# Optimization experiments

Measured on AMD Instinct MI355X. Metric: run time of the kernel, lower is better.

## Reference

```python
import jax, jax.numpy as jnp
import numpy as np

EPS = 1e-6

def _rmsnorm(x, w):
    rms = jax.lax.rsqrt(jnp.mean(x * x, axis=-1, keepdims=True) + EPS)
    return x * rms * w

def setup_inputs() -> dict:
    key = jax.random.key(0)
    ks = jax.random.split(key, 4)
    BS, N, D, DI = 4, 8192, 1024, 2048
    x = jax.random.normal(ks[0], (BS, N, D), dtype=jnp.float32)
    h_prev = jax.random.normal(ks[1], (BS, DI), dtype=jnp.float32)
    norm_w = jnp.ones((D,), dtype=jnp.float32)
    W_in = jax.random.normal(ks[2], (2 * DI, D), dtype=jnp.float32) * (1.0 / np.sqrt(D))
    b_in = jnp.zeros((2 * DI,), dtype=jnp.float32)
    W_out = jax.random.normal(ks[3], (D, DI), dtype=jnp.float32) * (1.0 / np.sqrt(DI))
    b_out = jnp.zeros((D,), dtype=jnp.float32)
    return {"x": x, "h_prev": h_prev, "norm_w": norm_w, "W_in": W_in,
            "b_in": b_in, "W_out": W_out, "b_out": b_out}

def _scan(a, b, h0):
    # h_t = a_t * h_{t-1} + b_t ; fold h0 into first step
    b = b.at[:, 0].set(a[:, 0] * h0 + b[:, 0])
    def combine(c1, c2):
        a1, b1 = c1
        a2, b2 = c2
        return (a2 * a1, a2 * b1 + b2)
    _, h = jax.lax.associative_scan(combine, (a, b), axis=1)
    return h  # [BS, N, E]

def reference(x, h_prev, norm_w, W_in, b_in, W_out, b_out):
    DI = W_out.shape[1]
    xn = _rmsnorm(x, norm_w)
    ab = jnp.einsum('bnd,ed->bne', xn, W_in) + b_in  # [BS, N, 2*DI]
    a_raw, b_raw = ab[..., :DI], ab[..., DI:]
    a = jax.nn.sigmoid(a_raw)
    b = jax.nn.silu(b_raw)
    h = _scan(a, b, h_prev)  # [BS, N, DI]
    out = jnp.einsum('bne,de->bnd', h, W_out) + b_out + x
    return out, h[:, -1]
```

## Files before the change

### kernel.cpp

```cpp
#include <hip/hip_runtime.h>
#include <stdint.h>
#include <stddef.h>

typedef __bf16 bf16;
typedef __attribute__((ext_vector_type(8))) __bf16 bf16x8;
typedef __attribute__((ext_vector_type(4))) __bf16 bf16x4;
typedef __attribute__((ext_vector_type(4))) float floatx4;

#define DEV static __device__ __forceinline__

DEV void async_load16(const void* g, void* l) {
  __builtin_amdgcn_global_load_lds(
      (__attribute__((address_space(1))) void*)(g),
      (__attribute__((address_space(3))) void*)(l),
      16, 0, 0);
}

DEV float bf16lo_to_f(uint32_t pv) {
  uint32_t b = pv << 16; float f; __builtin_memcpy(&f, &b, 4); return f;
}
DEV float bf16hi_to_f(uint32_t pv) {
  uint32_t b = pv & 0xffff0000u; float f; __builtin_memcpy(&f, &b, 4); return f;
}

DEV int win_orig_row(int c) {
  int jt16 = c >> 4;
  int is_b = jt16 & 1;
  int p    = (jt16 >> 1) * 16 + (c & 15);
  return p + is_b * 2048;
}

__global__ __launch_bounds__(256)
void f2bf_kernel(const float* __restrict__ in, bf16* __restrict__ out, int n4)
{
  int i = blockIdx.x * 256 + threadIdx.x;
  if (i < n4) {
    float4 v = ((const float4*)in)[i];
    bf16x4 o = { (bf16)v.x, (bf16)v.y, (bf16)v.z, (bf16)v.w };
    ((bf16x4*)out)[i] = o;
  }
}

__global__ __launch_bounds__(256)
void f2bf_win_perm(const float* __restrict__ in, bf16* __restrict__ out)
{
  int c = blockIdx.x;
  int orig = win_orig_row(c);
  float4 v = ((const float4*)(in + (size_t)orig * 1024))[threadIdx.x];
  bf16x4 o = { (bf16)v.x, (bf16)v.y, (bf16)v.z, (bf16)v.w };
  ((bf16x4*)(out + (size_t)c * 1024))[threadIdx.x] = o;
}

__global__ __launch_bounds__(256)
void bias_perm_kernel(const float* __restrict__ b_in, float* __restrict__ biasP)
{
  int c = blockIdx.x * 256 + threadIdx.x;
  biasP[c] = b_in[win_orig_row(c)];
}

__global__ __launch_bounds__(256)
void rmsnorm_kernel(const float* __restrict__ x, const float* __restrict__ w,
                    bf16* __restrict__ xn)
{
  const int row = blockIdx.x;
  const int tid = threadIdx.x;
  float4 v = ((const float4*)(x + (size_t)row * 1024))[tid];
  float ss = v.x * v.x + v.y * v.y + v.z * v.z + v.w * v.w;
  #pragma unroll
  for (int off = 1; off < 64; off <<= 1)
    ss += __shfl_xor(ss, off, 64);
  __shared__ float red[4];
  if ((tid & 63) == 0) red[tid >> 6] = ss;
  __syncthreads();
  float tot = red[0] + red[1] + red[2] + red[3];
  float rms = rsqrtf(tot * (1.0f / 1024.0f) + 1e-6f);
  float4 wv = ((const float4*)w)[tid];
  bf16x4 o;
  o[0] = (bf16)(v.x * rms * wv.x);
  o[1] = (bf16)(v.y * rms * wv.y);
  o[2] = (bf16)(v.z * rms * wv.z);
  o[3] = (bf16)(v.w * rms * wv.w);
  ((bf16x4*)(xn + (size_t)row * 1024))[tid] = o;
}

template <int MODE>
__global__ __launch_bounds__(256)
void gemm_bt_kernel(const bf16* __restrict__ A, const bf16* __restrict__ B,
                    int N, int K, int numNt,
                    uint32_t* __restrict__ sbw, float* __restrict__ out,
                    const float* __restrict__ bias,
                    const float* __restrict__ resid)
{
  __shared__ bf16 ldsA[128 * 64];
  __shared__ bf16 ldsB[128 * 64];

  const int GROUP_M = 16;
  int bid = blockIdx.x;
  int per_group = GROUP_M * numNt;
  int group = bid / per_group;
  int rem = bid - group * per_group;
  int mt = group * GROUP_M + (rem % GROUP_M);
  int nt = rem / GROUP_M;
  const int m0 = mt * 128, n0 = nt * 128;

  const int tid  = threadIdx.x;
  const int lane = tid & 63;
  const int wave = tid >> 6;
  const int wm   = (wave & 1) * 64;
  const int wn   = (wave >> 1) * 64;
  const int l15  = lane & 15;
  const int quad = lane >> 4;

  floatx4 acc[4][4];
  #pragma unroll
  for (int i = 0; i < 4; ++i)
    #pragma unroll
    for (int j = 0; j < 4; ++j)
      acc[i][j] = (floatx4){0.f, 0.f, 0.f, 0.f};

  for (int kt = 0; kt < K; kt += 64) {
    #pragma unroll
    for (int i = 0; i < 4; ++i) {
      int c   = tid + i * 256;
      int row = c >> 3;
      int kgg = (c & 7) ^ (row & 7);
      async_load16(A + (size_t)(m0 + row) * K + kt + kgg * 8, &ldsA[c * 8]);
      async_load16(B + (size_t)(n0 + row) * K + kt + kgg * 8, &ldsB[c * 8]);
    }
    __syncthreads();
    #pragma unroll
    for (int ks = 0; ks < 2; ++ks) {
      bf16x8 af[4], bfr[4];
      #pragma unroll
      for (int i = 0; i < 4; ++i) {
        int row = wm + i * 16 + l15;
        int kg  = ks * 4 + quad;
        af[i]  = *(const bf16x8*)&ldsA[(row * 8 + (kg ^ (row & 7))) * 8];
        int col = wn + i * 16 + l15;
        bfr[i] = *(const bf16x8*)&ldsB[(col * 8 + (kg ^ (col & 7))) * 8];
      }
      #pragma unroll
      for (int i = 0; i < 4; ++i)
        #pragma unroll
        for (int j = 0; j < 4; ++j)
          acc[i][j] = __builtin_amdgcn_mfma_f32_16x16x32_bf16(af[i], bfr[j], acc[i][j], 0, 0, 0);
    }
    __syncthreads();
  }

  if (MODE == 1) {
    #pragma unroll
    for (int i = 0; i < 4; ++i) {
      #pragma unroll
      for (int pair = 0; pair < 2; ++pair) {
        int j0 = pair * 2;
        float bs = bias[n0 + wn + j0 * 16 + l15];
        float bb = bias[n0 + wn + j0 * 16 + 16 + l15];
        int ch = (n0 >> 1) + (wn >> 1) + pair * 16 + l15;
        #pragma unroll
        for (int r = 0; r < 4; ++r) {
          int row = m0 + wm + i * 16 + quad * 4 + r;
          float vs = acc[i][j0][r] + bs;
          float vb = acc[i][j0 + 1][r] + bb;
          float s  = 1.0f / (1.0f + __expf(vs));
          float sv = 1.0f / (1.0f + __expf(vb));
          float bv = vb - vb * sv;
          union { bf16 h[2]; uint32_t u; } pk;
          pk.h[0] = (bf16)s;
          pk.h[1] = (bf16)bv;
          sbw[(size_t)row * 2048 + ch] = pk.u;
        }
      }
    }
  } else {
    #pragma unroll
    for (int i = 0; i < 4; ++i) {
      #pragma unroll
      for (int j = 0; j < 4; ++j) {
        #pragma unroll
        for (int r = 0; r < 4; ++r) {
          int row = m0 + wm + i * 16 + quad * 4 + r;
          int col = n0 + wn + j * 16 + l15;
          float v = acc[i][j][r] + bias[col] + resid[(size_t)row * N + col];
          out[(size_t)row * N + col] = v;
        }
      }
    }
  }
}

__global__ __launch_bounds__(256)
void scan_phase1(const uint32_t* __restrict__ sb,
                 float* __restrict__ Ac, float* __restrict__ Bc)
{
  int g = blockIdx.x * 256 + threadIdx.x;
  int e     = g & 2047;
  int chunk = (g >> 11) & 31;
  int seq   = g >> 16;
  size_t base = ((size_t)(seq * 8192 + chunk * 256)) * 2048 + e;
  float A = 1.0f, Bv = 0.0f;
  #pragma unroll 8
  for (int n = 0; n < 256; ++n) {
    uint32_t pv = sb[base + (size_t)n * 2048];
    float a = 1.0f - bf16lo_to_f(pv);
    float b = bf16hi_to_f(pv);
    A *= a;
    Bv = a * Bv + b;
  }
  Ac[g] = A;
  Bc[g] = Bv;
}

__global__ __launch_bounds__(256)
void scan_phase2(const float* __restrict__ Ac, const float* __restrict__ Bc,
                 const float* __restrict__ h_prev,
                 float* __restrict__ carry, float* __restrict__ h_last)
{
  int g = blockIdx.x * 256 + threadIdx.x;
  int e = g & 2047;
  int seq = g >> 11;
  float h = h_prev[g];
  #pragma unroll
  for (int c = 0; c < 32; ++c) {
    size_t idx = ((size_t)(seq * 32 + c)) * 2048 + e;
    carry[idx] = h;
    h = Ac[idx] * h + Bc[idx];
  }
  h_last[g] = h;
}

__global__ __launch_bounds__(256)
void scan_phase3(const uint32_t* __restrict__ sb,
                 const float* __restrict__ carry, bf16* __restrict__ h_out)
{
  int g = blockIdx.x * 256 + threadIdx.x;
  int e     = g & 2047;
  int chunk = (g >> 11) & 31;
  int seq   = g >> 16;
  float h = carry[((size_t)(seq * 32 + chunk)) * 2048 + e];
  size_t base = ((size_t)(seq * 8192 + chunk * 256)) * 2048 + e;
  #pragma unroll 8
  for (int n = 0; n < 256; ++n) {
    uint32_t pv = sb[base + (size_t)n * 2048];
    float a = 1.0f - bf16lo_to_f(pv);
    float b = bf16hi_to_f(pv);
    h = a * h + b;
    h_out[base + (size_t)n * 2048] = (bf16)h;
  }
}

extern "C" void kernel_launch(void* const* d_in, const int* in_sizes, int n_in,
                              void* d_out, int out_size, void* d_ws, size_t ws_size,
                              hipStream_t stream)
{
  const float* x      = (const float*)d_in[0];
  const float* h_prev = (const float*)d_in[1];
  const float* norm_w = (const float*)d_in[2];
  const float* W_in   = (const float*)d_in[3];
  const float* b_in   = (const float*)d_in[4];
  const float* W_out  = (const float*)d_in[5];
  const float* b_out  = (const float*)d_in[6];

  float* out    = (float*)d_out;
  float* h_last = out + (size_t)33554432;

  int BSl = 4, passes = 1;
  {
    size_t need4 = 8388608 + 4194304 + 16384
                 + 3 * ((size_t)4 * 32 * 2048 * 4)
                 + (size_t)4 * 8192 * 2048 * 4
                 + (size_t)4 * 8192 * 1024 * 2
                 + (size_t)4 * 8192 * 2048 * 2;
    if (ws_size < need4) { BSl = 1; passes = 4; }
  }
  const size_t Mrows = (size_t)BSl * 8192;
  char* ws = (char*)d_ws;
  bf16*  Win_b  = (bf16*)(ws);
  bf16*  Wout_b = (bf16*)(ws + 8388608);
  float* biasP  = (float*)(ws + 12582912);
  size_t acN    = (size_t)BSl * 32 * 2048;
  char*  pa     = ws + 12599296;
  float* Ac     = (float*)(pa);
  float* Bc     = (float*)(pa + acN * 4);
  float* carry  = (float*)(pa + acN * 8);
  char*  p0     = pa + acN * 12;
  uint32_t* sbw = (uint32_t*)(p0);
  bf16*  xn     = (bf16*)(p0 + Mrows * 2048 * 4);
  bf16*  h_arr  = (bf16*)(p0 + Mrows * 2048 * 4 + Mrows * 1024 * 2);

  f2bf_win_perm<<<4096, 256, 0, stream>>>(W_in, Win_b);
  f2bf_kernel<<<2048, 256, 0, stream>>>(W_out, Wout_b, 2097152 / 4);
  bias_perm_kernel<<<16, 256, 0, stream>>>(b_in, biasP);

  for (int p = 0; p < passes; ++p) {
    const float* xp = x + (size_t)p * Mrows * 1024;

    rmsnorm_kernel<<<(int)Mrows, 256, 0, stream>>>(xp, norm_w, xn);

    int numMt = (int)(Mrows / 128);
    gemm_bt_kernel<1><<<numMt * 32, 256, 0, stream>>>(
        xn, Win_b, 4096, 1024, 32, sbw, nullptr, biasP, nullptr);

    scan_phase1<<<BSl * 256, 256, 0, stream>>>(sbw, Ac, Bc);
    scan_phase2<<<BSl * 8, 256, 0, stream>>>(Ac, Bc, h_prev + (size_t)p * BSl * 2048,
                                             carry, h_last + (size_t)p * BSl * 2048);
    scan_phase3<<<BSl * 256, 256, 0, stream>>>(sbw, carry, h_arr);

    gemm_bt_kernel<2><<<numMt * 8, 256, 0, stream>>>(
        h_arr, Wout_b, 1024, 2048, 8, nullptr, out + (size_t)p * Mrows * 1024,
        b_out, xp);
  }
}
```

Before: 968.2 us.

## Replace 128x128 GEMM with 256x256 eight-wave pipelined double-buffered kernel

Both GEMMs move from a 128x128 tile with 4 waves and a single LDS buffer to a 256x256 tile with 8 waves. The new kernel double-buffers A and B in 128 KB of LDS and interleaves async global-to-LDS loads with MFMA quadrants under explicit waitcnt and barrier control plus s_setprio. Block IDs are also remapped across XCDs with a smaller M group. The aim is to hide load latency behind compute and raise arithmetic intensity per tile. In exchange it uses more registers and LDS, relies on fragile hand-written vmcnt accounting, and launches fewer blocks.

```diff
diff --git a/kernel.cpp b/kernel.cpp
--- a/kernel.cpp
+++ b/kernel.cpp
@@ -83,85 +83,175 @@
   ((bf16x4*)(xn + (size_t)row * 1024))[tid] = o;
 }
 
+DEV void stage_half(const bf16* __restrict__ P, int ldk, int grow0, int kt,
+                    bf16* ldst, int tid)
+{
+  #pragma unroll
+  for (int s = 0; s < 2; ++s) {
+    int cc  = (s << 9) + tid;
+    int row = cc >> 3;
+    int kgg = (cc & 7) ^ (row & 7);
+    async_load16(P + (size_t)(grow0 + row) * ldk + kt + kgg * 8, ldst + cc * 8);
+  }
+}
+
+DEV bf16x8 ld_frag(const bf16* base, int r, int kg) {
+  return *(const bf16x8*)(base + (((r << 3) + (kg ^ (r & 7))) << 3));
+}
+
+#define FENCE asm volatile("" ::: "memory")
+#define BAR() do { FENCE; __builtin_amdgcn_s_barrier(); FENCE; } while (0)
+#define LGKM0 asm volatile("s_waitcnt lgkmcnt(0)" ::: "memory")
+#define VMC4  asm volatile("s_waitcnt vmcnt(4)" ::: "memory")
+#define VMC0  asm volatile("s_waitcnt vmcnt(0)" ::: "memory")
+
+#define LOADA(LAP, IH) \
+  _Pragma("unroll") \
+  for (int ii = 0; ii < 4; ++ii) { \
+    _Pragma("unroll") \
+    for (int ks = 0; ks < 2; ++ks) \
+      af[ii][ks] = ld_frag(LAP, ((IH)*4 + ii)*16 + l15, ks*4 + quad); \
+  }
+
+#define LOADB(LBP, JH) \
+  _Pragma("unroll") \
+  for (int jj = 0; jj < 2; ++jj) { \
+    _Pragma("unroll") \
+    for (int ks = 0; ks < 2; ++ks) \
+      bfr[(JH)*2 + jj][ks] = ld_frag(LBP, rBb + ((JH)*2 + jj)*16 + l15, ks*4 + quad); \
+  }
+
+#define MFMAQ(IH, JH) \
+  _Pragma("unroll") \
+  for (int ii = 0; ii < 4; ++ii) { \
+    _Pragma("unroll") \
+    for (int jj = 0; jj < 2; ++jj) { \
+      _Pragma("unroll") \
+      for (int ks = 0; ks < 2; ++ks) \
+        acc[(IH)*4+ii][(JH)*2+jj] = __builtin_amdgcn_mfma_f32_16x16x32_bf16( \
+            af[ii][ks], bfr[(JH)*2+jj][ks], acc[(IH)*4+ii][(JH)*2+jj], 0, 0, 0); \
+    } \
+  }
+
 template <int MODE>
-__global__ __launch_bounds__(256)
-void gemm_bt_kernel(const bf16* __restrict__ A, const bf16* __restrict__ B,
+__global__ __launch_bounds__(512, 2)
+void gemm256_kernel(const bf16* __restrict__ A, const bf16* __restrict__ B,
                     int N, int K, int numNt,
                     uint32_t* __restrict__ sbw, float* __restrict__ out,
                     const float* __restrict__ bias,
                     const float* __restrict__ resid)
 {
-  __shared__ bf16 ldsA[128 * 64];
-  __shared__ bf16 ldsB[128 * 64];
-
-  const int GROUP_M = 16;
+  __shared__ __align__(16) bf16 lds[65536];
+
+  int nwg = gridDim.x;
   int bid = blockIdx.x;
+  int cpx = nwg >> 3;
+  int wg  = (bid & 7) * cpx + (bid >> 3);
+  const int GROUP_M = 8;
   int per_group = GROUP_M * numNt;
-  int group = bid / per_group;
-  int rem = bid - group * per_group;
+  int group = wg / per_group;
+  int rem   = wg - group * per_group;
   int mt = group * GROUP_M + (rem % GROUP_M);
   int nt = rem / GROUP_M;
-  const int m0 = mt * 128, n0 = nt * 128;
+  const int m0 = mt * 256, n0 = nt * 256;
 
   const int tid  = threadIdx.x;
   const int lane = tid & 63;
   const int wave = tid >> 6;
-  const int wm   = (wave & 1) * 64;
-  const int wn   = (wave >> 1) * 64;
+  const int wm   = wave >> 2;
+  const int wn   = wave & 3;
+  const int wh   = wn >> 1;
+  const int rBb  = (wn & 1) * 64;
   const int l15  = lane & 15;
   const int quad = lane >> 4;
 
-  floatx4 acc[4][4];
+  const bf16* lA0 = lds +         wm * 8192;
+  const bf16* lA1 = lds + 16384 + wm * 8192;
+  const bf16* lB0 = lds + 32768 + wh * 8192;
+  const bf16* lB1 = lds + 49152 + wh * 8192;
+
+  floatx4 acc[8][4];
   #pragma unroll
-  for (int i = 0; i < 4; ++i)
+  for (int i = 0; i < 8; ++i)
     #pragma unroll
     for (int j = 0; j < 4; ++j)
       acc[i][j] = (floatx4){0.f, 0.f, 0.f, 0.f};
 
-  for (int kt = 0; kt < K; kt += 64) {
-    #pragma unroll
-    for (int i = 0; i < 4; ++i) {
-      int c   = tid + i * 256;
-      int row = c >> 3;
-      int kgg = (c & 7) ^ (row & 7);
-      async_load16(A + (size_t)(m0 + row) * K + kt + kgg * 8, &ldsA[c * 8]);
-      async_load16(B + (size_t)(n0 + row) * K + kt + kgg * 8, &ldsB[c * 8]);
-    }
-    __syncthreads();
-    #pragma unroll
-    for (int ks = 0; ks < 2; ++ks) {
-      bf16x8 af[4], bfr[4];
-      #pragma unroll
-      for (int i = 0; i < 4; ++i) {
-        int row = wm + i * 16 + l15;
-        int kg  = ks * 4 + quad;
-        af[i]  = *(const bf16x8*)&ldsA[(row * 8 + (kg ^ (row & 7))) * 8];
-        int col = wn + i * 16 + l15;
-        bfr[i] = *(const bf16x8*)&ldsB[(col * 8 + (kg ^ (col & 7))) * 8];
-      }
-      #pragma unroll
-      for (int i = 0; i < 4; ++i)
-        #pragma unroll
-        for (int j = 0; j < 4; ++j)
-          acc[i][j] = __builtin_amdgcn_mfma_f32_16x16x32_bf16(af[i], bfr[j], acc[i][j], 0, 0, 0);
-    }
-    __syncthreads();
+  bf16x8 af[4][2];
+  bf16x8 bfr[4][2];
+
+  stage_half(A, K, m0,       0, lds +     0, tid);
+  stage_half(A, K, m0 + 128, 0, lds +  8192, tid);
+  stage_half(B, K, n0,       0, lds + 32768, tid);
+  stage_half(B, K, n0 + 128, 0, lds + 40960, tid);
+  stage_half(B, K, n0,      64, lds + 49152, tid);
+  stage_half(B, K, n0 + 128,64, lds + 57344, tid);
+  VMC4;
+  BAR();
+
+  const int U = K >> 7;
+  for (int u = 0; u < U; ++u) {
+    const int k1 = (u << 7) + 64;
+    const int k2 = (u << 7) + 128;
+    const int k3 = (u << 7) + 192;
+    const bool more = (u + 1 < U);
+
+    LOADA(lA0, 0); LOADB(lB0, 0);
+    stage_half(A, K, m0, k1, lds + 16384, tid);
+    BAR(); LGKM0;
+    __builtin_amdgcn_s_setprio(1); MFMAQ(0, 0); __builtin_amdgcn_s_setprio(0);
+    BAR();
+    LOADB(lB0, 1);
+    stage_half(A, K, m0 + 128, k1, lds + 24576, tid);
+    BAR(); LGKM0;
+    __builtin_amdgcn_s_setprio(1); MFMAQ(0, 1); __builtin_amdgcn_s_setprio(0);
+    BAR();
+    LOADA(lA0, 1);
+    if (more) stage_half(B, K, n0, k2, lds + 32768, tid);
+    BAR(); LGKM0;
+    __builtin_amdgcn_s_setprio(1); MFMAQ(1, 0); __builtin_amdgcn_s_setprio(0);
+    BAR();
+    if (more) stage_half(B, K, n0 + 128, k2, lds + 40960, tid);
+    BAR(); LGKM0;
+    __builtin_amdgcn_s_setprio(1); MFMAQ(1, 1); __builtin_amdgcn_s_setprio(0);
+    if (more) { VMC4; } else { VMC0; }
+    BAR();
+    LOADA(lA1, 0); LOADB(lB1, 0);
+    if (more) stage_half(A, K, m0, k2, lds + 0, tid);
+    BAR(); LGKM0;
+    __builtin_amdgcn_s_setprio(1); MFMAQ(0, 0); __builtin_amdgcn_s_setprio(0);
+    BAR();
+    LOADB(lB1, 1);
+    if (more) stage_half(A, K, m0 + 128, k2, lds + 8192, tid);
+    BAR(); LGKM0;
+    __builtin_amdgcn_s_setprio(1); MFMAQ(0, 1); __builtin_amdgcn_s_setprio(0);
+    BAR();
+    LOADA(lA1, 1);
+    if (more) stage_half(B, K, n0, k3, lds + 49152, tid);
+    BAR(); LGKM0;
+    __builtin_amdgcn_s_setprio(1); MFMAQ(1, 0); __builtin_amdgcn_s_setprio(0);
+    BAR();
+    if (more) stage_half(B, K, n0 + 128, k3, lds + 57344, tid);
+    BAR(); LGKM0;
+    __builtin_amdgcn_s_setprio(1); MFMAQ(1, 1); __builtin_amdgcn_s_setprio(0);
+    if (more) VMC4;
+    BAR();
   }
 
   if (MODE == 1) {
     #pragma unroll
-    for (int i = 0; i < 4; ++i) {
+    for (int i = 0; i < 8; ++i) {
       #pragma unroll
       for (int pair = 0; pair < 2; ++pair) {
-        int j0 = pair * 2;
-        float bs = bias[n0 + wn + j0 * 16 + l15];
-        float bb = bias[n0 + wn + j0 * 16 + 16 + l15];
-        int ch = (n0 >> 1) + (wn >> 1) + pair * 16 + l15;
+        int colb = n0 + wn * 64 + pair * 32;
+        float bs = bias[colb + l15];
+        float bb = bias[colb + 16 + l15];
+        int ch = (colb >> 5) * 16 + l15;
         #pragma unroll
         for (int r = 0; r < 4; ++r) {
-          int row = m0 + wm + i * 16 + quad * 4 + r;
-          float vs = acc[i][j0][r] + bs;
-          float vb = acc[i][j0 + 1][r] + bb;
+          int row = m0 + wm * 128 + i * 16 + quad * 4 + r;
+          float vs = acc[i][pair * 2][r] + bs;
+          float vb = acc[i][pair * 2 + 1][r] + bb;
           float s  = 1.0f / (1.0f + __expf(vs));
           float sv = 1.0f / (1.0f + __expf(vb));
           float bv = vb - vb * sv;
@@ -174,14 +264,15 @@
     }
   } else {
     #pragma unroll
-    for (int i = 0; i < 4; ++i) {
+    for (int i = 0; i < 8; ++i) {
       #pragma unroll
       for (int j = 0; j < 4; ++j) {
+        int col = n0 + wn * 64 + j * 16 + l15;
+        float bc = bias[col];
         #pragma unroll
         for (int r = 0; r < 4; ++r) {
-          int row = m0 + wm + i * 16 + quad * 4 + r;
-          int col = n0 + wn + j * 16 + l15;
-          float v = acc[i][j][r] + bias[col] + resid[(size_t)row * N + col];
+          int row = m0 + wm * 128 + i * 16 + quad * 4 + r;
+          float v = acc[i][j][r] + bc + resid[(size_t)row * N + col];
           out[(size_t)row * N + col] = v;
         }
       }
@@ -297,17 +388,17 @@
 
     rmsnorm_kernel<<<(int)Mrows, 256, 0, stream>>>(xp, norm_w, xn);
 
-    int numMt = (int)(Mrows / 128);
-    gemm_bt_kernel<1><<<numMt * 32, 256, 0, stream>>>(
-        xn, Win_b, 4096, 1024, 32, sbw, nullptr, biasP, nullptr);
+    int numMt = (int)(Mrows / 256);
+    gemm256_kernel<1><<<numMt * 16, 512, 0, stream>>>(
+        xn, Win_b, 4096, 1024, 16, sbw, nullptr, biasP, nullptr);
 
     scan_phase1<<<BSl * 256, 256, 0, stream>>>(sbw, Ac, Bc);
     scan_phase2<<<BSl * 8, 256, 0, stream>>>(Ac, Bc, h_prev + (size_t)p * BSl * 2048,
                                              carry, h_last + (size_t)p * BSl * 2048);
     scan_phase3<<<BSl * 256, 256, 0, stream>>>(sbw, carry, h_arr);
 
-    gemm_bt_kernel<2><<<numMt * 8, 256, 0, stream>>>(
-        h_arr, Wout_b, 1024, 2048, 8, nullptr, out + (size_t)p * Mrows * 1024,
+    gemm256_kernel<2><<<numMt * 4, 512, 0, stream>>>(
+        h_arr, Wout_b, 1024, 2048, 4, nullptr, out + (size_t)p * Mrows * 1024,
         b_out, xp);
   }
 }
```

New measurement: 800.0 us. 17.4% less time.
